# Optimization experiments

Measured on AMD Instinct MI355X. Metric: run time of the kernel, lower is better.

Reference implementation:

```python
import jax, jax.numpy as jnp
import numpy as np


def setup_inputs() -> dict:
    key = jax.random.key(0)
    ks = jax.random.split(key, 5)
    B, S, H, I = 8, 2048, 1024, 4096
    # int8 quantized activation / weights / int8 bias, held as int32 for portability
    hidden_states = jax.random.randint(ks[0], (B, S, H), -128, 128, dtype=jnp.int32)
    w_fc = jax.random.randint(ks[1], (H, I), -128, 128, dtype=jnp.int32)   # Conv1D weight [in, out]
    b_fc = jax.random.randint(ks[2], (I,), -128, 128, dtype=jnp.int32)     # int8 bias (B8)
    w_proj = jax.random.randint(ks[3], (I, H), -128, 128, dtype=jnp.int32)
    b_proj = jax.random.normal(ks[4], (H,), dtype=jnp.float32)             # fp32 bias (BFP32)
    alpha_fc = jnp.float32(0.004)   # (x_scale * w_scale / out_scale) of c_fc
    beta_fc = jnp.float32(0.02)     # bias_scale / out_scale of c_fc
    alpha_proj = jnp.float32(0.003) # x_scale * w_scale of c_proj (dequant to fp32)
    return {
        "hidden_states": hidden_states,
        "w_fc": w_fc, "b_fc": b_fc, "alpha_fc": alpha_fc, "beta_fc": beta_fc,
        "w_proj": w_proj, "b_proj": b_proj, "alpha_proj": alpha_proj,
    }


def reference(hidden_states, w_fc, b_fc, alpha_fc, beta_fc, w_proj, b_proj, alpha_proj):
    # ---- c_fc: W8A8B8O8 Conv1D + fused ReLU + requantization to int8 ----
    acc1 = jnp.matmul(hidden_states, w_fc)                       # [B,S,I] int32
    h = acc1.astype(jnp.float32) * alpha_fc + b_fc.astype(jnp.float32) * beta_fc
    h = jax.nn.relu(h)
    # requantize to int8 (round + saturate)
    h_q = jnp.clip(jnp.round(h), -128.0, 127.0).astype(jnp.int32)  # [B,S,I]
    # ---- c_proj: W8A8BFP32OFP32 Conv1D (dequant to fp32) ----
    acc2 = jnp.matmul(h_q, w_proj)                               # [B,S,H] int32
    out = acc2.astype(jnp.float32) * alpha_proj + b_proj
    # dropout is identity in eval mode
    return out
```

## Files before the change

kernel.cpp:

```cpp
#include <hip/hip_runtime.h>
#include <cstdint>
#include <cstddef>

typedef int int4v __attribute__((ext_vector_type(4)));
typedef signed char schar;

#define DEVI __device__ __forceinline__

DEVI void load_lds16(const void* g, void* l) {
  __builtin_amdgcn_global_load_lds(
      (const __attribute__((address_space(1))) void*)g,
      (__attribute__((address_space(3))) void*)l, 16, 0, 0);
}

#define SB0() __builtin_amdgcn_sched_barrier(0)
#define BAR() __builtin_amdgcn_s_barrier()
#define LGKM(n)                                                   \
  do {                                                            \
    asm volatile("s_waitcnt lgkmcnt(" #n ")" ::: "memory");       \
    SB0();                                                        \
  } while (0)
#define VMW(n)                                                    \
  do {                                                            \
    asm volatile("s_waitcnt vmcnt(" #n ")" ::: "memory");         \
    SB0();                                                        \
  } while (0)

__global__ __launch_bounds__(256) void pack_i8(const int* __restrict__ src,
                                               signed char* __restrict__ dst,
                                               int n4) {
  int i = blockIdx.x * 256 + threadIdx.x;
  if (i >= n4) return;
  int4v v = ((const int4v*)src)[i];
  int p = (v.x & 255) | ((v.y & 255) << 8) | ((v.z & 255) << 16) | (v.w << 24);
  ((int*)dst)[i] = p;
}

__global__ __launch_bounds__(256) void pack_wT(const int* __restrict__ w,
                                               signed char* __restrict__ wT,
                                               int K, int N) {
  __shared__ signed char t[64][68];
  int n0 = blockIdx.x * 64, k0 = blockIdx.y * 64;
  int tr = threadIdx.x >> 6, tc = threadIdx.x & 63;
#pragma unroll
  for (int i = 0; i < 16; ++i) {
    int r = i * 4 + tr;
    t[r][tc] = (signed char)w[(size_t)(k0 + r) * N + n0 + tc];
  }
  __syncthreads();
#pragma unroll
  for (int i = 0; i < 16; ++i) {
    int r = i * 4 + tr;
    wT[(size_t)(n0 + r) * K + k0 + tc] = t[tc][r];
  }
}

template <int EPI>
__global__ __launch_bounds__(512, 2) void gemmP(
    const schar* __restrict__ A, const schar* __restrict__ BT,
    int M, int N, int K, const int* __restrict__ bias_i,
    const float* __restrict__ alphaP, const float* __restrict__ betaP,
    const float* __restrict__ bias_f, schar* __restrict__ outQ,
    float* __restrict__ outF) {
  extern __shared__ schar lds[];

  const int tid = threadIdx.x;
  const int wid = tid >> 6, lane = tid & 63;
  const int wr = wid >> 2, wc = wid & 3;
  const int l16 = lane & 15, l4 = lane >> 4;

  const int gx = gridDim.x;
  const int nwg = gx * gridDim.y;
  const int bid = blockIdx.y * gx + blockIdx.x;
  const int swz = (bid & 7) * (nwg >> 3) + (bid >> 3);
  const int rowBase = (swz / gx) * 256;
  const int colBase = (swz % gx) * 256;
  const int NT = K >> 6;

  const float alpha = alphaP[0];
  const float beta = (EPI == 0) ? betaP[0] : 0.f;
  asm volatile("" ::"s"(alpha), "s"(beta));
  LGKM(0);

  const schar* gA[2];
  const schar* gB[2];
#pragma unroll
  for (int c = 0; c < 2; ++c) {
    int o = c * 8192 + tid * 16;
    int r = o >> 6;
    int g = ((o >> 4) & 3) ^ ((r >> 1) & 3);
    gA[c] = A + (size_t)(rowBase + r) * K + g * 16;
    gB[c] = BT + (size_t)(colBase + r) * K + g * 16;
  }

  auto stage = [&](int buf, int t) {
    schar* d = lds + buf * 32768 + wid * 1024;
    load_lds16(gA[0] + (size_t)t * 64, d);
    load_lds16(gA[1] + (size_t)t * 64, d + 8192);
    load_lds16(gB[0] + (size_t)t * 64, d + 16384);
    load_lds16(gB[1] + (size_t)t * 64, d + 24576);
  };

  const int slotc = (l4 ^ ((l16 >> 1) & 3)) * 16 + l16 * 64;

  int4v acc[8][4] = {};
  int4v aF[8], bF[4];

#define RDA(Ab)                                                   \
  _Pragma("unroll") for (int mi = 0; mi < 8; ++mi) aF[mi] =       \
      *(const int4v*)((Ab) + wr * 8192 + mi * 1024 + slotc)
#define RDB(Bb)                                                   \
  _Pragma("unroll") for (int ni = 0; ni < 4; ++ni) bF[ni] =       \
      *(const int4v*)((Bb) + wc * 4096 + ni * 1024 + slotc)
#define MMALL()                                                        \
  do {                                                                 \
    __builtin_amdgcn_s_setprio(1);                                     \
    _Pragma("unroll") for (int mi = 0; mi < 8; ++mi)                   \
        _Pragma("unroll") for (int ni = 0; ni < 4; ++ni) acc[mi][ni] = \
        __builtin_amdgcn_mfma_i32_16x16x64_i8(aF[mi], bF[ni],          \
                                              acc[mi][ni], 0, 0, 0);   \
    __builtin_amdgcn_s_setprio(0);                                     \
  } while (0)

  stage(0, 0);
  stage(1, 1);
  VMW(4);
  BAR();

  for (int T = 0; T < NT; ++T) {
    const int cb = T & 3;
    const schar* Ab = lds + cb * 32768;
    const schar* Bb = Ab + 16384;

    if (T + 2 < NT) stage((T + 2) & 3, T + 2);
    RDA(Ab);
    RDB(Bb);
    MMALL();

    LGKM(0);
    if (T + 2 < NT) {
      VMW(4);
    } else {
      VMW(0);
    }
    BAR();
  }

  if (EPI == 0) {
#pragma unroll
    for (int MI = 0; MI < 8; ++MI) {
      int row = rowBase + wr * 128 + MI * 16 + l4 * 4;
#pragma unroll
      for (int NI = 0; NI < 4; ++NI) {
        int col = colBase + wc * 64 + NI * 16 + l16;
        float bt = (float)bias_i[col] * beta;
#pragma unroll
        for (int j = 0; j < 4; ++j) {
          float h = (float)acc[MI][NI][j] * alpha + bt;
          h = fmaxf(h, 0.f);
          h = rintf(h);
          h = fminf(h, 127.f);
          outQ[(size_t)(row + j) * N + col] = (schar)h;
        }
      }
    }
  } else {
#pragma unroll
    for (int MI = 0; MI < 8; ++MI) {
      int row = rowBase + wr * 128 + MI * 16 + l4 * 4;
#pragma unroll
      for (int NI = 0; NI < 4; ++NI) {
        int col = colBase + wc * 64 + NI * 16 + l16;
        float bv = bias_f[col];
#pragma unroll
        for (int j = 0; j < 4; ++j)
          outF[(size_t)(row + j) * N + col] =
              (float)acc[MI][NI][j] * alpha + bv;
      }
    }
  }
#undef RDA
#undef RDB
#undef MMALL
}

extern "C" void kernel_launch(void* const* d_in, const int* in_sizes, int n_in,
                              void* d_out, int out_size, void* d_ws,
                              size_t ws_size, hipStream_t stream) {
  const int M = 16384, H = 1024, I = 4096;
  const int* hidden = (const int*)d_in[0];
  const int* w_fc = (const int*)d_in[1];
  const int* b_fc = (const int*)d_in[2];
  const float* alpha_fc = (const float*)d_in[3];
  const float* beta_fc = (const float*)d_in[4];
  const int* w_proj = (const int*)d_in[5];
  const float* b_proj = (const float*)d_in[6];
  const float* alpha_proj = (const float*)d_in[7];
  float* out = (float*)d_out;

  signed char* hq = (signed char*)d_ws;
  signed char* aP = hq + (size_t)M * I;
  signed char* wfcT = aP + (size_t)M * H;
  signed char* wpT = wfcT + (size_t)I * H;

  hipFuncSetAttribute((const void*)gemmP<0>,
                      hipFuncAttributeMaxDynamicSharedMemorySize, 131072);
  hipFuncSetAttribute((const void*)gemmP<1>,
                      hipFuncAttributeMaxDynamicSharedMemorySize, 131072);

  pack_i8<<<(M * H / 4 + 255) / 256, 256, 0, stream>>>(hidden, aP, M * H / 4);
  pack_wT<<<dim3(I / 64, H / 64), 256, 0, stream>>>(w_fc, wfcT, H, I);
  pack_wT<<<dim3(H / 64, I / 64), 256, 0, stream>>>(w_proj, wpT, I, H);

  gemmP<0><<<dim3(I / 256, M / 256), 512, 131072, stream>>>(
      aP, wfcT, M, I, H, b_fc, alpha_fc, beta_fc, nullptr, hq, nullptr);
  gemmP<1><<<dim3(H / 256, M / 256), 512, 131072, stream>>>(
      hq, wpT, M, H, I, nullptr, alpha_proj, nullptr, b_proj, nullptr, out);
}
```

Baseline: 187.1 us.

## Deepen LDS prefetch to three stages and interleave fragment reads with MFMAs

The int8 GEMM main loop now stages three K-tiles ahead into the 4-slot LDS ring instead of two. A fragments are double-buffered in registers, so the next tile's A reads are issued while the current tile's MFMA quads run. Each tile is split into four 4x2 MFMA quads with B fragment reads interleaved between them, and the loop is unrolled by two. The sched_barrier and memory clobbers on the waitcnt asm were removed, which gives the compiler more freedom to reorder but risks LDS reads moving past the intended sync points and raises register pressure.

```diff
diff --git a/kernel.cpp b/kernel.cpp
--- a/kernel.cpp
+++ b/kernel.cpp
@@ -13,18 +13,9 @@
       (__attribute__((address_space(3))) void*)l, 16, 0, 0);
 }
 
-#define SB0() __builtin_amdgcn_sched_barrier(0)
 #define BAR() __builtin_amdgcn_s_barrier()
-#define LGKM(n)                                                   \
-  do {                                                            \
-    asm volatile("s_waitcnt lgkmcnt(" #n ")" ::: "memory");       \
-    SB0();                                                        \
-  } while (0)
-#define VMW(n)                                                    \
-  do {                                                            \
-    asm volatile("s_waitcnt vmcnt(" #n ")" ::: "memory");         \
-    SB0();                                                        \
-  } while (0)
+#define LGKM(n) asm volatile("s_waitcnt lgkmcnt(" #n ")")
+#define VMW(n) asm volatile("s_waitcnt vmcnt(" #n ")")
 
 __global__ __launch_bounds__(256) void pack_i8(const int* __restrict__ src,
                                                signed char* __restrict__ dst,
@@ -56,7 +47,7 @@
 }
 
 template <int EPI>
-__global__ __launch_bounds__(512, 2) void gemmP(
+__global__ __launch_bounds__(512, 2) void gemmW(
     const schar* __restrict__ A, const schar* __restrict__ BT,
     int M, int N, int K, const int* __restrict__ bias_i,
     const float* __restrict__ alphaP, const float* __restrict__ betaP,
@@ -102,48 +93,72 @@
   };
 
   const int slotc = (l4 ^ ((l16 >> 1) & 3)) * 16 + l16 * 64;
+  const int aoff = wr * 8192 + slotc;
+  const int boff = 16384 + wc * 4096 + slotc;
 
   int4v acc[8][4] = {};
-  int4v aF[8], bF[4];
-
-#define RDA(Ab)                                                   \
-  _Pragma("unroll") for (int mi = 0; mi < 8; ++mi) aF[mi] =       \
-      *(const int4v*)((Ab) + wr * 8192 + mi * 1024 + slotc)
-#define RDB(Bb)                                                   \
-  _Pragma("unroll") for (int ni = 0; ni < 4; ++ni) bF[ni] =       \
-      *(const int4v*)((Bb) + wc * 4096 + ni * 1024 + slotc)
-#define MMALL()                                                        \
+  int4v aA0[4], aB0[4], aA1[4], aB1[4];
+  int4v b0[2], b1[2];
+
+#define RD_AH(DST, Ab)                                            \
+  _Pragma("unroll") for (int f = 0; f < 4; ++f) (DST)[f] =        \
+      *(const int4v*)((Ab) + aoff + f * 1024)
+#define RD_AL(DST, Ab)                                            \
+  _Pragma("unroll") for (int f = 0; f < 4; ++f) (DST)[f] =        \
+      *(const int4v*)((Ab) + aoff + (4 + f) * 1024)
+#define RD_B(DST, Bb, N0)                                         \
+  _Pragma("unroll") for (int n = 0; n < 2; ++n) (DST)[n] =        \
+      *(const int4v*)((Bb) + boff + ((N0) + n) * 1024)
+#define QUAD(AF, M0, BF, N0)                                           \
   do {                                                                 \
     __builtin_amdgcn_s_setprio(1);                                     \
-    _Pragma("unroll") for (int mi = 0; mi < 8; ++mi)                   \
-        _Pragma("unroll") for (int ni = 0; ni < 4; ++ni) acc[mi][ni] = \
-        __builtin_amdgcn_mfma_i32_16x16x64_i8(aF[mi], bF[ni],          \
-                                              acc[mi][ni], 0, 0, 0);   \
+    _Pragma("unroll") for (int mi = 0; mi < 4; ++mi)                   \
+        _Pragma("unroll") for (int ni = 0; ni < 2; ++ni)               \
+            acc[(M0) + mi][(N0) + ni] =                                \
+        __builtin_amdgcn_mfma_i32_16x16x64_i8(                         \
+            (AF)[mi], (BF)[ni], acc[(M0) + mi][(N0) + ni], 0, 0, 0);   \
     __builtin_amdgcn_s_setprio(0);                                     \
   } while (0)
 
+#define TILE(T, cA, cB, nA, nB)                                        \
+  do {                                                                 \
+    const int tt = (T);                                                \
+    const schar* buf = lds + (tt & 3) * 32768;                         \
+    const schar* bufn = lds + ((tt + 1) & 3) * 32768;                  \
+                                   \
+    if (tt + 3 < NT) stage((tt + 3) & 3, tt + 3);                      \
+    RD_B(b0, buf, 0);                                                  \
+    LGKM(0);                                                           \
+    QUAD(cA, 0, b0, 0);                                                \
+                                                  \
+    RD_B(b1, buf, 2);                                                  \
+    LGKM(0);                                                           \
+    QUAD(cB, 4, b0, 0);                                                \
+         \
+    if (tt + 1 < NT) RD_AH(nA, bufn);                                  \
+    QUAD(cA, 0, b1, 2);                                                \
+                                  \
+    if (tt + 1 < NT) RD_AL(nB, bufn);                                  \
+    QUAD(cB, 4, b1, 2);                                                \
+    if (tt + 3 < NT) {                                                 \
+      VMW(4);      \
+    } else {                                                           \
+      VMW(0);                           \
+    }                                                                  \
+    BAR();                                                             \
+  } while (0)
+
   stage(0, 0);
   stage(1, 1);
-  VMW(4);
+  stage(2, 2);
+  VMW(8);
   BAR();
-
-  for (int T = 0; T < NT; ++T) {
-    const int cb = T & 3;
-    const schar* Ab = lds + cb * 32768;
-    const schar* Bb = Ab + 16384;
-
-    if (T + 2 < NT) stage((T + 2) & 3, T + 2);
-    RDA(Ab);
-    RDB(Bb);
-    MMALL();
-
-    LGKM(0);
-    if (T + 2 < NT) {
-      VMW(4);
-    } else {
-      VMW(0);
-    }
-    BAR();
+  RD_AH(aA0, lds);
+  RD_AL(aB0, lds);
+
+  for (int T = 0; T < NT; T += 2) {
+    TILE(T, aA0, aB0, aA1, aB1);
+    TILE(T + 1, aA1, aB1, aA0, aB0);
   }
 
   if (EPI == 0) {
@@ -179,9 +194,11 @@
       }
     }
   }
-#undef RDA
-#undef RDB
-#undef MMALL
+#undef RD_AH
+#undef RD_AL
+#undef RD_B
+#undef QUAD
+#undef TILE
 }
 
 extern "C" void kernel_launch(void* const* d_in, const int* in_sizes, int n_in,
@@ -203,17 +220,17 @@
   signed char* wfcT = aP + (size_t)M * H;
   signed char* wpT = wfcT + (size_t)I * H;
 
-  hipFuncSetAttribute((const void*)gemmP<0>,
+  hipFuncSetAttribute((const void*)gemmW<0>,
                       hipFuncAttributeMaxDynamicSharedMemorySize, 131072);
-  hipFuncSetAttribute((const void*)gemmP<1>,
+  hipFuncSetAttribute((const void*)gemmW<1>,
                       hipFuncAttributeMaxDynamicSharedMemorySize, 131072);
 
   pack_i8<<<(M * H / 4 + 255) / 256, 256, 0, stream>>>(hidden, aP, M * H / 4);
   pack_wT<<<dim3(I / 64, H / 64), 256, 0, stream>>>(w_fc, wfcT, H, I);
   pack_wT<<<dim3(H / 64, I / 64), 256, 0, stream>>>(w_proj, wpT, I, H);
 
-  gemmP<0><<<dim3(I / 256, M / 256), 512, 131072, stream>>>(
+  gemmW<0><<<dim3(I / 256, M / 256), 512, 131072, stream>>>(
       aP, wfcT, M, I, H, b_fc, alpha_fc, beta_fc, nullptr, hq, nullptr);
-  gemmP<1><<<dim3(H / 256, M / 256), 512, 131072, stream>>>(
+  gemmW<1><<<dim3(H / 256, M / 256), 512, 131072, stream>>>(
       hq, wpT, M, H, I, nullptr, alpha_proj, nullptr, b_proj, nullptr, out);
 }
```

Measured after the change: 189.8 us. About the same (+1.4%).

## Load B fragments directly from global into registers, stage only A in LDS

Applied to the files above, without the earlier changes.

The B operand is no longer staged through LDS. Each wave now reads its B fragments straight from global memory into registers every K-step, and only A is staged via global_load_lds, which halves LDS use to 64KB. This cuts LDS traffic and LDS capacity pressure but exposes per-iteration global load latency for B with no prefetch. It also removes the sched_barrier from the waitcnt macros, which lets the compiler reorder around the waits.

```diff
diff --git a/kernel.cpp b/kernel.cpp
--- a/kernel.cpp
+++ b/kernel.cpp
@@ -13,18 +13,9 @@
       (__attribute__((address_space(3))) void*)l, 16, 0, 0);
 }
 
-#define SB0() __builtin_amdgcn_sched_barrier(0)
 #define BAR() __builtin_amdgcn_s_barrier()
-#define LGKM(n)                                                   \
-  do {                                                            \
-    asm volatile("s_waitcnt lgkmcnt(" #n ")" ::: "memory");       \
-    SB0();                                                        \
-  } while (0)
-#define VMW(n)                                                    \
-  do {                                                            \
-    asm volatile("s_waitcnt vmcnt(" #n ")" ::: "memory");         \
-    SB0();                                                        \
-  } while (0)
+#define LGKM(n) asm volatile("s_waitcnt lgkmcnt(" #n ")")
+#define VMW(n) asm volatile("s_waitcnt vmcnt(" #n ")")
 
 __global__ __launch_bounds__(256) void pack_i8(const int* __restrict__ src,
                                                signed char* __restrict__ dst,
@@ -56,7 +47,7 @@
 }
 
 template <int EPI>
-__global__ __launch_bounds__(512, 2) void gemmP(
+__global__ __launch_bounds__(512, 2) void gemmD(
     const schar* __restrict__ A, const schar* __restrict__ BT,
     int M, int N, int K, const int* __restrict__ bias_i,
     const float* __restrict__ alphaP, const float* __restrict__ betaP,
@@ -83,63 +74,62 @@
   LGKM(0);
 
   const schar* gA[2];
-  const schar* gB[2];
 #pragma unroll
   for (int c = 0; c < 2; ++c) {
     int o = c * 8192 + tid * 16;
     int r = o >> 6;
     int g = ((o >> 4) & 3) ^ ((r >> 1) & 3);
     gA[c] = A + (size_t)(rowBase + r) * K + g * 16;
-    gB[c] = BT + (size_t)(colBase + r) * K + g * 16;
-  }
-
-  auto stage = [&](int buf, int t) {
-    schar* d = lds + buf * 32768 + wid * 1024;
+  }
+  auto stageA = [&](int buf, int t) {
+    schar* d = lds + buf * 16384 + wid * 1024;
     load_lds16(gA[0] + (size_t)t * 64, d);
     load_lds16(gA[1] + (size_t)t * 64, d + 8192);
-    load_lds16(gB[0] + (size_t)t * 64, d + 16384);
-    load_lds16(gB[1] + (size_t)t * 64, d + 24576);
   };
 
+  const schar* gBp[4];
+#pragma unroll
+  for (int ni = 0; ni < 4; ++ni)
+    gBp[ni] =
+        BT + (size_t)(colBase + wc * 64 + ni * 16 + l16) * K + l4 * 16;
+
   const int slotc = (l4 ^ ((l16 >> 1) & 3)) * 16 + l16 * 64;
+  const int aoff = wr * 8192 + slotc;
 
   int4v acc[8][4] = {};
-  int4v aF[8], bF[4];
-
-#define RDA(Ab)                                                   \
-  _Pragma("unroll") for (int mi = 0; mi < 8; ++mi) aF[mi] =       \
-      *(const int4v*)((Ab) + wr * 8192 + mi * 1024 + slotc)
-#define RDB(Bb)                                                   \
-  _Pragma("unroll") for (int ni = 0; ni < 4; ++ni) bF[ni] =       \
-      *(const int4v*)((Bb) + wc * 4096 + ni * 1024 + slotc)
-#define MMALL()                                                        \
-  do {                                                                 \
-    __builtin_amdgcn_s_setprio(1);                                     \
-    _Pragma("unroll") for (int mi = 0; mi < 8; ++mi)                   \
-        _Pragma("unroll") for (int ni = 0; ni < 4; ++ni) acc[mi][ni] = \
-        __builtin_amdgcn_mfma_i32_16x16x64_i8(aF[mi], bF[ni],          \
-                                              acc[mi][ni], 0, 0, 0);   \
-    __builtin_amdgcn_s_setprio(0);                                     \
-  } while (0)
-
-  stage(0, 0);
-  stage(1, 1);
-  VMW(4);
+
+  stageA(0, 0);
+  stageA(1, 1);
+  VMW(0);
   BAR();
 
   for (int T = 0; T < NT; ++T) {
-    const int cb = T & 3;
-    const schar* Ab = lds + cb * 32768;
-    const schar* Bb = Ab + 16384;
-
-    if (T + 2 < NT) stage((T + 2) & 3, T + 2);
-    RDA(Ab);
-    RDB(Bb);
-    MMALL();
+    const schar* Ab = lds + (T & 3) * 16384;
+
+    int4v bF[4];
+#pragma unroll
+    for (int ni = 0; ni < 4; ++ni)
+      bF[ni] = *(const int4v*)(gBp[ni] + (size_t)T * 64);
+
+    if (T + 2 < NT) stageA((T + 2) & 3, T + 2);
+
+    int4v aF[8];
+#pragma unroll
+    for (int f = 0; f < 8; ++f)
+      aF[f] = *(const int4v*)(Ab + aoff + f * 1024);
+
+    __builtin_amdgcn_s_setprio(1);
+#pragma unroll
+    for (int mi = 0; mi < 8; ++mi)
+#pragma unroll
+      for (int ni = 0; ni < 4; ++ni)
+        acc[mi][ni] = __builtin_amdgcn_mfma_i32_16x16x64_i8(
+            aF[mi], bF[ni], acc[mi][ni], 0, 0, 0);
+    __builtin_amdgcn_s_setprio(0);
 
     LGKM(0);
     if (T + 2 < NT) {
-      VMW(4);
+      VMW(2);
     } else {
       VMW(0);
     }
@@ -179,9 +169,6 @@
       }
     }
   }
-#undef RDA
-#undef RDB
-#undef MMALL
 }
 
 extern "C" void kernel_launch(void* const* d_in, const int* in_sizes, int n_in,
@@ -203,17 +190,17 @@
   signed char* wfcT = aP + (size_t)M * H;
   signed char* wpT = wfcT + (size_t)I * H;
 
-  hipFuncSetAttribute((const void*)gemmP<0>,
-                      hipFuncAttributeMaxDynamicSharedMemorySize, 131072);
-  hipFuncSetAttribute((const void*)gemmP<1>,
-                      hipFuncAttributeMaxDynamicSharedMemorySize, 131072);
+  hipFuncSetAttribute((const void*)gemmD<0>,
+                      hipFuncAttributeMaxDynamicSharedMemorySize, 65536);
+  hipFuncSetAttribute((const void*)gemmD<1>,
+                      hipFuncAttributeMaxDynamicSharedMemorySize, 65536);
 
   pack_i8<<<(M * H / 4 + 255) / 256, 256, 0, stream>>>(hidden, aP, M * H / 4);
   pack_wT<<<dim3(I / 64, H / 64), 256, 0, stream>>>(w_fc, wfcT, H, I);
   pack_wT<<<dim3(H / 64, I / 64), 256, 0, stream>>>(w_proj, wpT, I, H);
 
-  gemmP<0><<<dim3(I / 256, M / 256), 512, 131072, stream>>>(
+  gemmD<0><<<dim3(I / 256, M / 256), 512, 65536, stream>>>(
       aP, wfcT, M, I, H, b_fc, alpha_fc, beta_fc, nullptr, hq, nullptr);
-  gemmP<1><<<dim3(H / 256, M / 256), 512, 131072, stream>>>(
+  gemmD<1><<<dim3(H / 256, M / 256), 512, 65536, stream>>>(
       hq, wpT, M, H, I, nullptr, alpha_proj, nullptr, b_proj, nullptr, out);
 }
```

Measured after the change: 261.1 us. +39.5%, slower.

## Restructure int8 GEMM to 1024-thread blocks with K=128 double-buffered tiles

Applied to the files above, without the earlier changes.

Reworks the int8 MFMA GEMM to use 16 waves per 256x256 tile (4x4 wave grid, 64x64 per wave) instead of 8 waves, with one block per CU. K-step doubles to 128 with an 8-way XOR LDS swizzle, and the pipeline drops from a 4-buffer, two-tile prefetch to two buffers with one tile of prefetch. The goal is more waves per CU to hide latency and fewer barriers per K. The cost is a shallower prefetch, a full vmcnt(0) wait every iteration, and sched_barrier fences removed from the waits, so the compiler may reorder around them.

```diff
diff --git a/kernel.cpp b/kernel.cpp
--- a/kernel.cpp
+++ b/kernel.cpp
@@ -13,18 +13,9 @@
       (__attribute__((address_space(3))) void*)l, 16, 0, 0);
 }
 
-#define SB0() __builtin_amdgcn_sched_barrier(0)
 #define BAR() __builtin_amdgcn_s_barrier()
-#define LGKM(n)                                                   \
-  do {                                                            \
-    asm volatile("s_waitcnt lgkmcnt(" #n ")" ::: "memory");       \
-    SB0();                                                        \
-  } while (0)
-#define VMW(n)                                                    \
-  do {                                                            \
-    asm volatile("s_waitcnt vmcnt(" #n ")" ::: "memory");         \
-    SB0();                                                        \
-  } while (0)
+#define LGKM(n) asm volatile("s_waitcnt lgkmcnt(" #n ")")
+#define VMW(n) asm volatile("s_waitcnt vmcnt(" #n ")")
 
 __global__ __launch_bounds__(256) void pack_i8(const int* __restrict__ src,
                                                signed char* __restrict__ dst,
@@ -56,7 +47,7 @@
 }
 
 template <int EPI>
-__global__ __launch_bounds__(512, 2) void gemmP(
+__global__ __launch_bounds__(1024, 1) void gemmT(
     const schar* __restrict__ A, const schar* __restrict__ BT,
     int M, int N, int K, const int* __restrict__ bias_i,
     const float* __restrict__ alphaP, const float* __restrict__ betaP,
@@ -75,7 +66,7 @@
   const int swz = (bid & 7) * (nwg >> 3) + (bid >> 3);
   const int rowBase = (swz / gx) * 256;
   const int colBase = (swz % gx) * 256;
-  const int NT = K >> 6;
+  const int NT = K >> 7;
 
   const float alpha = alphaP[0];
   const float beta = (EPI == 0) ? betaP[0] : 0.f;
@@ -86,36 +77,39 @@
   const schar* gB[2];
 #pragma unroll
   for (int c = 0; c < 2; ++c) {
-    int o = c * 8192 + tid * 16;
-    int r = o >> 6;
-    int g = ((o >> 4) & 3) ^ ((r >> 1) & 3);
+    int o = c * 16384 + tid * 16;
+    int r = o >> 7;
+    int g = ((o >> 4) & 7) ^ (r & 7);
     gA[c] = A + (size_t)(rowBase + r) * K + g * 16;
     gB[c] = BT + (size_t)(colBase + r) * K + g * 16;
   }
-
   auto stage = [&](int buf, int t) {
-    schar* d = lds + buf * 32768 + wid * 1024;
-    load_lds16(gA[0] + (size_t)t * 64, d);
-    load_lds16(gA[1] + (size_t)t * 64, d + 8192);
-    load_lds16(gB[0] + (size_t)t * 64, d + 16384);
-    load_lds16(gB[1] + (size_t)t * 64, d + 24576);
+    schar* dA = lds + buf * 32768 + wid * 1024;
+    schar* dB = lds + 65536 + buf * 32768 + wid * 1024;
+    load_lds16(gA[0] + (size_t)t * 128, dA);
+    load_lds16(gA[1] + (size_t)t * 128, dA + 16384);
+    load_lds16(gB[0] + (size_t)t * 128, dB);
+    load_lds16(gB[1] + (size_t)t * 128, dB + 16384);
   };
 
-  const int slotc = (l4 ^ ((l16 >> 1) & 3)) * 16 + l16 * 64;
-
-  int4v acc[8][4] = {};
-  int4v aF[8], bF[4];
-
-#define RDA(Ab)                                                   \
-  _Pragma("unroll") for (int mi = 0; mi < 8; ++mi) aF[mi] =       \
-      *(const int4v*)((Ab) + wr * 8192 + mi * 1024 + slotc)
-#define RDB(Bb)                                                   \
+  const int so0 = ((0 + l4) ^ (l16 & 7)) * 16 + l16 * 128;
+  const int so1 = ((4 + l4) ^ (l16 & 7)) * 16 + l16 * 128;
+  const int aoff = wr * 8192;
+  const int boff = wc * 8192;
+
+  int4v acc[4][4] = {};
+  int4v aF[4], bF[4];
+
+#define RDA(SO, Ab)                                               \
+  _Pragma("unroll") for (int mi = 0; mi < 4; ++mi) aF[mi] =       \
+      *(const int4v*)((Ab) + aoff + mi * 2048 + (SO))
+#define RDB(SO, Bb)                                               \
   _Pragma("unroll") for (int ni = 0; ni < 4; ++ni) bF[ni] =       \
-      *(const int4v*)((Bb) + wc * 4096 + ni * 1024 + slotc)
+      *(const int4v*)((Bb) + boff + ni * 2048 + (SO))
 #define MMALL()                                                        \
   do {                                                                 \
     __builtin_amdgcn_s_setprio(1);                                     \
-    _Pragma("unroll") for (int mi = 0; mi < 8; ++mi)                   \
+    _Pragma("unroll") for (int mi = 0; mi < 4; ++mi)                   \
         _Pragma("unroll") for (int ni = 0; ni < 4; ++ni) acc[mi][ni] = \
         __builtin_amdgcn_mfma_i32_16x16x64_i8(aF[mi], bF[ni],          \
                                               acc[mi][ni], 0, 0, 0);   \
@@ -123,33 +117,33 @@
   } while (0)
 
   stage(0, 0);
-  stage(1, 1);
-  VMW(4);
+  VMW(0);
   BAR();
 
   for (int T = 0; T < NT; ++T) {
-    const int cb = T & 3;
+    const int cb = T & 1;
     const schar* Ab = lds + cb * 32768;
-    const schar* Bb = Ab + 16384;
-
-    if (T + 2 < NT) stage((T + 2) & 3, T + 2);
-    RDA(Ab);
-    RDB(Bb);
+    const schar* Bb = lds + 65536 + cb * 32768;
+
+    if (T + 1 < NT) stage(cb ^ 1, T + 1);
+
+    RDA(so0, Ab);
+    RDB(so0, Bb);
+    LGKM(0);
     MMALL();
-
+    RDA(so1, Ab);
+    RDB(so1, Bb);
     LGKM(0);
-    if (T + 2 < NT) {
-      VMW(4);
-    } else {
-      VMW(0);
-    }
+    MMALL();
+
+    VMW(0);
     BAR();
   }
 
   if (EPI == 0) {
 #pragma unroll
-    for (int MI = 0; MI < 8; ++MI) {
-      int row = rowBase + wr * 128 + MI * 16 + l4 * 4;
+    for (int MI = 0; MI < 4; ++MI) {
+      int row = rowBase + wr * 64 + MI * 16 + l4 * 4;
 #pragma unroll
       for (int NI = 0; NI < 4; ++NI) {
         int col = colBase + wc * 64 + NI * 16 + l16;
@@ -166,8 +160,8 @@
     }
   } else {
 #pragma unroll
-    for (int MI = 0; MI < 8; ++MI) {
-      int row = rowBase + wr * 128 + MI * 16 + l4 * 4;
+    for (int MI = 0; MI < 4; ++MI) {
+      int row = rowBase + wr * 64 + MI * 16 + l4 * 4;
 #pragma unroll
       for (int NI = 0; NI < 4; ++NI) {
         int col = colBase + wc * 64 + NI * 16 + l16;
@@ -203,17 +197,17 @@
   signed char* wfcT = aP + (size_t)M * H;
   signed char* wpT = wfcT + (size_t)I * H;
 
-  hipFuncSetAttribute((const void*)gemmP<0>,
+  hipFuncSetAttribute((const void*)gemmT<0>,
                       hipFuncAttributeMaxDynamicSharedMemorySize, 131072);
-  hipFuncSetAttribute((const void*)gemmP<1>,
+  hipFuncSetAttribute((const void*)gemmT<1>,
                       hipFuncAttributeMaxDynamicSharedMemorySize, 131072);
 
   pack_i8<<<(M * H / 4 + 255) / 256, 256, 0, stream>>>(hidden, aP, M * H / 4);
   pack_wT<<<dim3(I / 64, H / 64), 256, 0, stream>>>(w_fc, wfcT, H, I);
   pack_wT<<<dim3(H / 64, I / 64), 256, 0, stream>>>(w_proj, wpT, I, H);
 
-  gemmP<0><<<dim3(I / 256, M / 256), 512, 131072, stream>>>(
+  gemmT<0><<<dim3(I / 256, M / 256), 1024, 131072, stream>>>(
       aP, wfcT, M, I, H, b_fc, alpha_fc, beta_fc, nullptr, hq, nullptr);
-  gemmP<1><<<dim3(H / 256, M / 256), 512, 131072, stream>>>(
+  gemmT<1><<<dim3(H / 256, M / 256), 1024, 131072, stream>>>(
       hq, wpT, M, H, I, nullptr, alpha_proj, nullptr, b_proj, nullptr, out);
 }
```

Result: faster. 173.4 us (-7.3%).
